# Kernel tuning notes

Hardware: AMD Instinct MI355X
Metric: run time of the kernel (lower is better)

Reference implementation:

```python
import jax, jax.numpy as jnp
import numpy as np

CAT_SIZES = [31360, 6807, 18, 94]
TOTAL = int(sum(CAT_SIZES))          # 38279
EMB = 128
N_FIELDS = len(CAT_SIZES)
D_IN = N_FIELDS * EMB                # 512 (num_features is empty)
MLP_DIMS = [2048, 1024, 512]
B = 16384
OFFSETS = np.concatenate([[0], np.cumsum(CAT_SIZES)[:-1]]).astype(np.int32)


def setup_inputs() -> dict:
    key = jax.random.key(0)
    ks = jax.random.split(key, 20)
    # x holds raw per-field category ids stored as float32 (as the torch model expects)
    cols = [jax.random.randint(ks[i], (B,), 0, s) for i, s in enumerate(CAT_SIZES)]
    x = jnp.stack(cols, axis=1).astype(jnp.float32)

    bias = jnp.zeros((1,), jnp.float32)
    fc = jax.random.uniform(ks[4], (TOTAL, 1), dtype=jnp.float32)          # nn.Parameter(torch.rand)
    emb_table = jax.random.normal(ks[5], (TOTAL, EMB), dtype=jnp.float32)  # nn.Embedding default N(0,1)

    dims = [D_IN] + MLP_DIMS + [1]
    params = {}
    for i in range(len(dims) - 1):
        fan_in = dims[i]
        bound = 1.0 / np.sqrt(fan_in)
        params[f"W{i+1}"] = jax.random.uniform(ks[6 + 2 * i], (dims[i], dims[i + 1]), jnp.float32, -bound, bound)
        params[f"b{i+1}"] = jax.random.uniform(ks[7 + 2 * i], (dims[i + 1],), jnp.float32, -bound, bound)

    return dict(x=x, bias=bias, fc=fc, emb_table=emb_table, **params)


def reference(x, bias, fc, emb_table, W1, b1, W2, b2, W3, b3, W4, b4):
    cat = x.astype(jnp.int32)                       # [B, F] raw per-field ids
    b = cat.shape[0]

    # embedding lookup with RAW (un-offset) ids, faithful to the original code
    embed_x = emb_table[cat].reshape(b, -1)          # [B, F*EMB]

    # one_hot(offset ids) @ fc  ==  sum_f fc[offset ids]  (offset ranges disjoint)
    gidx = cat + jnp.asarray(OFFSETS)                # [B, F] global ids
    lin = jnp.sum(fc[gidx, 0], axis=1)               # [B]
    fm_y = bias + lin                                # [B]

    # FM term: embed_x is 2-D, so sum over dim=1 collapses features;
    # the keepdim sum over dim=-1 then collapses the BATCH dim to shape (1,)
    # (a quirk of the original code that we reproduce exactly)
    square_of_sum = jnp.sum(embed_x, axis=1) ** 2    # [B]
    sum_of_square = jnp.sum(embed_x ** 2, axis=1)    # [B]
    fm_y = fm_y + 0.5 * jnp.sum(square_of_sum - sum_of_square, axis=-1, keepdims=True)  # [B]
    fm_y = fm_y[:, None]                             # [B,1]

    # MLP (eval mode: dropout is identity)
    h = embed_x
    for W, bb in ((W1, b1), (W2, b2), (W3, b3)):
        h = jax.nn.relu(h @ W + bb)
    mlp_y = h @ W4 + b4                              # [B,1]

    return jax.nn.sigmoid(fm_y + mlp_y)              # [B,1]
```

## Files before the change

kernel.cpp:

```cpp
#include <hip/hip_runtime.h>
#include <hip/hip_fp8.h>
#include <cstdint>


typedef float f32x4 __attribute__((ext_vector_type(4)));
typedef int i32x4 __attribute__((ext_vector_type(4)));
typedef int i32x8 __attribute__((ext_vector_type(8)));

#define GLOAD16(gptr, lptr)                                                \
  __builtin_amdgcn_global_load_lds(                                        \
      (const __attribute__((address_space(1))) void*)(gptr),               \
      (__attribute__((address_space(3))) void*)(lptr), 16, 0, 0)

__device__ inline uint32_t f2fp4(float v) {
  uint32_t s = (__float_as_uint(v) >> 31) << 3;
  float a = fabsf(v);
  uint32_t m;
  if (a < 0.25f) m = 0;
  else if (a < 0.75f) m = 1;
  else if (a < 1.25f) m = 2;
  else if (a < 1.75f) m = 3;
  else if (a < 2.5f)  m = 4;
  else if (a < 3.5f)  m = 5;
  else if (a < 5.0f)  m = 6;
  else m = 7;
  return s | m;
}

static constexpr size_t OFF_LIN  = 0;
static constexpr size_t OFF_PART = 65536;
static constexpr size_t OFF_ACC  = 98304;
static constexpr size_t OFF_EMB  = 262144;
static constexpr size_t OFF_H1   = OFF_EMB + 8388608ull;
static constexpr size_t OFF_H2   = OFF_H1 + 33554432ull;
static constexpr size_t OFF_W1T  = OFF_H2 + 16777216ull;
static constexpr size_t OFF_W2T  = OFF_W1T + 524288ull;
static constexpr size_t OFF_W3T  = OFF_W2T + 1048576ull;

__global__ void prep(const float* __restrict__ W1, const float* __restrict__ W2,
                     const float* __restrict__ W3, uint8_t* __restrict__ W1T,
                     uint8_t* __restrict__ W2T, uint8_t* __restrict__ W3T,
                     const float* __restrict__ x, const float* __restrict__ fc,
                     const float* __restrict__ emb, uint8_t* __restrict__ ebf,
                     float* __restrict__ lin, float* __restrict__ partials,
                     float* __restrict__ dotacc) {
  __shared__ __align__(16) float smem[32 * 33];
  int blk = blockIdx.x;
  int tid = threadIdx.x;
  if (blk < 3584) {
    const float* W;
    uint8_t* WT;
    int K, N, bx, by;
    if (blk < 1024) {
      W = W1; WT = W1T; K = 512; N = 2048; bx = blk & 63; by = blk >> 6;
    } else if (blk < 3072) {
      int t = blk - 1024;
      W = W2; WT = W2T; K = 2048; N = 1024; bx = t & 31; by = t >> 5;
    } else {
      int t = blk - 3072;
      W = W3; WT = W3T; K = 1024; N = 512; bx = t & 15; by = t >> 4;
    }
    int tx = tid & 31, ty = tid >> 5;
    int n0 = bx * 32, k0 = by * 32;
#pragma unroll
    for (int i = ty; i < 32; i += 8)
      smem[i * 33 + tx] = W[(size_t)(k0 + i) * N + n0 + tx];
    __syncthreads();
    if (tx < 16) {
#pragma unroll
      for (int i = ty; i < 32; i += 8) {
        uint32_t lo = f2fp4(smem[(2 * tx) * 33 + i] * 128.f);
        uint32_t hi = f2fp4(smem[(2 * tx + 1) * 33 + i] * 128.f);
        WT[(size_t)(n0 + i) * (K >> 1) + (k0 >> 1) + tx] =
            (uint8_t)(lo | (hi << 4));
      }
    }
  } else if (blk < 7680) {
    int gb = blk - 3584;
    int wv = tid >> 6, lane = tid & 63;
    int b = gb * 4 + wv;
    int f = lane >> 4;
    int idx = (int)x[b * 4 + f];
    const float* row = emb + (size_t)idx * 128 + (lane & 15) * 8;
    float4 v0 = ((const float4*)row)[0];
    float4 v1 = ((const float4*)row)[1];
    float s = v0.x + v0.y + v0.z + v0.w + v1.x + v1.y + v1.z + v1.w;
    float q = v0.x * v0.x + v0.y * v0.y + v0.z * v0.z + v0.w * v0.w +
              v1.x * v1.x + v1.y * v1.y + v1.z * v1.z + v1.w * v1.w;

    int lo = 0, hi = 0;
    lo = __builtin_amdgcn_cvt_pk_fp8_f32(v0.x, v0.y, lo, false);
    lo = __builtin_amdgcn_cvt_pk_fp8_f32(v0.z, v0.w, lo, true);
    hi = __builtin_amdgcn_cvt_pk_fp8_f32(v1.x, v1.y, hi, false);
    hi = __builtin_amdgcn_cvt_pk_fp8_f32(v1.z, v1.w, hi, true);
    int2 pk = make_int2(lo, hi);
    *(int2*)(ebf + (size_t)b * 512 + lane * 8) = pk;

    float lp = 0.f;
    if ((lane & 15) == 0) {
      int off = (f == 1) ? 31360 : (f == 2) ? 38167 : (f == 3) ? 38185 : 0;
      lp = fc[idx + off];
    }
#pragma unroll
    for (int m = 32; m; m >>= 1) {
      s += __shfl_xor(s, m);
      q += __shfl_xor(q, m);
      lp += __shfl_xor(lp, m);
    }
    float* pt = smem;
    if (lane == 0) {
      lin[b] = lp;
      pt[wv] = s * s - q;
    }
    __syncthreads();
    if (tid == 0) partials[gb] = pt[0] + pt[1] + pt[2] + pt[3];
  } else {
    int zb = blk - 7680;
    ((float4*)dotacc)[zb * 256 + tid] = make_float4(0.f, 0.f, 0.f, 0.f);
  }
}

__global__ __launch_bounds__(256) void gemm_mx_relu(
    const uint8_t* __restrict__ A, const uint8_t* __restrict__ BT,
    const float* __restrict__ bias, uint8_t* __restrict__ C, int K, int N,
    int GX) {
  __shared__ __align__(16) uint8_t As[128][128];
  __shared__ __align__(16) uint8_t Bs[128][64];
  int bid = blockIdx.x;
  int by = (bid & 7) + ((bid >> 3) / GX) * 8;
  int bx = (bid >> 3) & (GX - 1);
  int tid = threadIdx.x;
  int wv = tid >> 6, lane = tid & 63;
  int m0 = by * 128, n0 = bx * 128;
  int mw = (wv >> 1) * 64, nw = (wv & 1) * 64;
  int ml = lane & 15, kg = lane >> 4;
  int Kb2 = K >> 1;
  int asrow = lane >> 3;
  int ascol = ((lane & 7) ^ asrow) * 16;
  int bsrow = lane >> 2;
  int bscol = ((lane & 3) ^ (bsrow & 3)) * 16;
  int pa0 = ((2 * kg) ^ (ml & 7)) * 16;
  int pa1 = ((2 * kg + 1) ^ (ml & 7)) * 16;
  int pb = (kg ^ (ml & 3)) * 16;

  f32x4 acc[4][4];
#pragma unroll
  for (int i = 0; i < 4; ++i)
#pragma unroll
    for (int j = 0; j < 4; ++j) acc[i][j] = (f32x4){0.f, 0.f, 0.f, 0.f};

  for (int kt = 0; kt < K; kt += 128) {
#pragma unroll
    for (int r = 0; r < 4; ++r) {
      int g = r * 4 + wv;
      const uint8_t* ga = A + (size_t)(m0 + 8 * g + asrow) * K + kt + ascol;
      GLOAD16(ga, &As[8 * g][0]);
    }
#pragma unroll
    for (int r = 0; r < 2; ++r) {
      int g = r * 4 + wv;
      const uint8_t* gb =
          BT + (size_t)(n0 + 16 * g + bsrow) * Kb2 + (kt >> 1) + bscol;
      GLOAD16(gb, &Bs[16 * g][0]);
    }
    __syncthreads();

    i32x4 z = (i32x4){0, 0, 0, 0};
    i32x8 af[4], bfr[4];
#pragma unroll
    for (int t = 0; t < 4; ++t) {
      int ra = mw + t * 16 + ml;
      i32x4 a0 = *(const i32x4*)&As[ra][pa0];
      i32x4 a1 = *(const i32x4*)&As[ra][pa1];
      af[t] = __builtin_shufflevector(a0, a1, 0, 1, 2, 3, 4, 5, 6, 7);
      i32x4 vb = *(const i32x4*)&Bs[nw + t * 16 + ml][pb];
      bfr[t] = __builtin_shufflevector(vb, z, 0, 1, 2, 3, 4, 5, 6, 7);
    }
#pragma unroll
    for (int mt = 0; mt < 4; ++mt)
#pragma unroll
      for (int nt = 0; nt < 4; ++nt)
        acc[mt][nt] = __builtin_amdgcn_mfma_scale_f32_16x16x128_f8f6f4(
            af[mt], bfr[nt], acc[mt][nt],
             0,  4,
            0, 0x7F7F7F7F, 0, 0x78787878);
    __syncthreads();
  }

  int rbase = kg * 4;
#pragma unroll
  for (int nt = 0; nt < 4; ++nt) {
    int col = n0 + nw + nt * 16 + ml;
    float bv = bias[col];
#pragma unroll
    for (int mt = 0; mt < 4; ++mt) {
      int row = m0 + mw + mt * 16 + rbase;
      float v0 = acc[mt][nt][0] + bv, v1 = acc[mt][nt][1] + bv;
      float v2 = acc[mt][nt][2] + bv, v3 = acc[mt][nt][3] + bv;
      v0 = v0 > 0.f ? v0 : 0.f;
      v1 = v1 > 0.f ? v1 : 0.f;
      v2 = v2 > 0.f ? v2 : 0.f;
      v3 = v3 > 0.f ? v3 : 0.f;
      int w01 = __builtin_amdgcn_cvt_pk_fp8_f32(v0, v1, 0, false);
      int w23 = __builtin_amdgcn_cvt_pk_fp8_f32(v2, v3, 0, false);
      C[(size_t)(row + 0) * N + col] = (uint8_t)(w01 & 0xFF);
      C[(size_t)(row + 1) * N + col] = (uint8_t)((w01 >> 8) & 0xFF);
      C[(size_t)(row + 2) * N + col] = (uint8_t)(w23 & 0xFF);
      C[(size_t)(row + 3) * N + col] = (uint8_t)((w23 >> 8) & 0xFF);
    }
  }
}

__global__ __launch_bounds__(256) void gemm_mx_dot(
    const uint8_t* __restrict__ A, const uint8_t* __restrict__ BT,
    const float* __restrict__ bias, const float* __restrict__ W4,
    float* __restrict__ dotacc, int K, int N, int GX) {
  __shared__ __align__(16) uint8_t As[128][128];
  __shared__ __align__(16) uint8_t Bs[128][64];
  int bid = blockIdx.x;
  int by = (bid & 7) + ((bid >> 3) / GX) * 8;
  int bx = (bid >> 3) & (GX - 1);
  int tid = threadIdx.x;
  int wv = tid >> 6, lane = tid & 63;
  int m0 = by * 128, n0 = bx * 128;
  int mw = (wv >> 1) * 64, nw = (wv & 1) * 64;
  int ml = lane & 15, kg = lane >> 4;
  int Kb2 = K >> 1;
  int asrow = lane >> 3;
  int ascol = ((lane & 7) ^ asrow) * 16;
  int bsrow = lane >> 2;
  int bscol = ((lane & 3) ^ (bsrow & 3)) * 16;
  int pa0 = ((2 * kg) ^ (ml & 7)) * 16;
  int pa1 = ((2 * kg + 1) ^ (ml & 7)) * 16;
  int pb = (kg ^ (ml & 3)) * 16;

  f32x4 acc[4][4];
#pragma unroll
  for (int i = 0; i < 4; ++i)
#pragma unroll
    for (int j = 0; j < 4; ++j) acc[i][j] = (f32x4){0.f, 0.f, 0.f, 0.f};

  for (int kt = 0; kt < K; kt += 128) {
#pragma unroll
    for (int r = 0; r < 4; ++r) {
      int g = r * 4 + wv;
      const uint8_t* ga = A + (size_t)(m0 + 8 * g + asrow) * K + kt + ascol;
      GLOAD16(ga, &As[8 * g][0]);
    }
#pragma unroll
    for (int r = 0; r < 2; ++r) {
      int g = r * 4 + wv;
      const uint8_t* gb =
          BT + (size_t)(n0 + 16 * g + bsrow) * Kb2 + (kt >> 1) + bscol;
      GLOAD16(gb, &Bs[16 * g][0]);
    }
    __syncthreads();

    i32x4 z = (i32x4){0, 0, 0, 0};
    i32x8 af[4], bfr[4];
#pragma unroll
    for (int t = 0; t < 4; ++t) {
      int ra = mw + t * 16 + ml;
      i32x4 a0 = *(const i32x4*)&As[ra][pa0];
      i32x4 a1 = *(const i32x4*)&As[ra][pa1];
      af[t] = __builtin_shufflevector(a0, a1, 0, 1, 2, 3, 4, 5, 6, 7);
      i32x4 vb = *(const i32x4*)&Bs[nw + t * 16 + ml][pb];
      bfr[t] = __builtin_shufflevector(vb, z, 0, 1, 2, 3, 4, 5, 6, 7);
    }
#pragma unroll
    for (int mt = 0; mt < 4; ++mt)
#pragma unroll
      for (int nt = 0; nt < 4; ++nt)
        acc[mt][nt] = __builtin_amdgcn_mfma_scale_f32_16x16x128_f8f6f4(
            af[mt], bfr[nt], acc[mt][nt],
            0, 4, 0, 0x7F7F7F7F, 0, 0x78787878);
    __syncthreads();
  }

  float bv[4], w4v[4];
#pragma unroll
  for (int nt = 0; nt < 4; ++nt) {
    int col = n0 + nw + nt * 16 + ml;
    bv[nt] = bias[col];
    w4v[nt] = W4[col];
  }
  int rbase = kg * 4;
#pragma unroll
  for (int mt = 0; mt < 4; ++mt) {
#pragma unroll
    for (int r = 0; r < 4; ++r) {
      float p = 0.f;
#pragma unroll
      for (int nt = 0; nt < 4; ++nt) {
        float v = acc[mt][nt][r] + bv[nt];
        v = v > 0.f ? v : 0.f;
        p += v * w4v[nt];
      }
#pragma unroll
      for (int m = 1; m < 16; m <<= 1) p += __shfl_xor(p, m);
      if (ml == 0)
        atomicAdd(&dotacc[m0 + mw + mt * 16 + rbase + r], p);
    }
  }
}

__global__ void final_out(const float* __restrict__ part,
                          const float* __restrict__ dotacc,
                          const float* __restrict__ lin,
                          const float* __restrict__ bias,
                          const float* __restrict__ b4,
                          float* __restrict__ out) {
  __shared__ float ps[4];
  int tid = threadIdx.x;
  float v = 0.f;
  for (int i = tid; i < 4096; i += 256) v += part[i];
#pragma unroll
  for (int m = 32; m; m >>= 1) v += __shfl_xor(v, m);
  if ((tid & 63) == 0) ps[tid >> 6] = v;
  __syncthreads();
  float S = ps[0] + ps[1] + ps[2] + ps[3];
  int i = blockIdx.x * 256 + tid;
  float z = dotacc[i] + b4[0] + bias[0] + lin[i] + 0.5f * S;
  out[i] = 1.f / (1.f + expf(-z));
}

extern "C" void kernel_launch(void* const* d_in, const int* in_sizes, int n_in,
                              void* d_out, int out_size, void* d_ws,
                              size_t ws_size, hipStream_t stream) {
  const float* x    = (const float*)d_in[0];
  const float* bias = (const float*)d_in[1];
  const float* fc   = (const float*)d_in[2];
  const float* emb  = (const float*)d_in[3];
  const float* W1   = (const float*)d_in[4];
  const float* b1   = (const float*)d_in[5];
  const float* W2   = (const float*)d_in[6];
  const float* b2   = (const float*)d_in[7];
  const float* W3   = (const float*)d_in[8];
  const float* b3   = (const float*)d_in[9];
  const float* W4   = (const float*)d_in[10];
  const float* b4   = (const float*)d_in[11];
  float* out = (float*)d_out;

  char* ws = (char*)d_ws;
  float* lin    = (float*)(ws + OFF_LIN);
  float* part   = (float*)(ws + OFF_PART);
  float* dacc   = (float*)(ws + OFF_ACC);
  uint8_t* EMBb = (uint8_t*)(ws + OFF_EMB);
  uint8_t* H1   = (uint8_t*)(ws + OFF_H1);
  uint8_t* H2   = (uint8_t*)(ws + OFF_H2);
  uint8_t* W1T  = (uint8_t*)(ws + OFF_W1T);
  uint8_t* W2T  = (uint8_t*)(ws + OFF_W2T);
  uint8_t* W3T  = (uint8_t*)(ws + OFF_W3T);

  prep<<<7696, 256, 0, stream>>>(W1, W2, W3, W1T, W2T, W3T, x, fc, emb, EMBb,
                                 lin, part, dacc);

  gemm_mx_relu<<<2048, 256, 0, stream>>>(EMBb, W1T, b1, H1, 512, 2048, 16);
  gemm_mx_relu<<<1024, 256, 0, stream>>>(H1, W2T, b2, H2, 2048, 1024, 8);
  gemm_mx_dot<<<512, 256, 0, stream>>>(H2, W3T, b3, W4, dacc, 1024, 512, 4);

  final_out<<<64, 256, 0, stream>>>(part, dacc, lin, bias, b4, out);
}
```

Baseline: 179.9 us.

## Double-buffer LDS tiles in MX GEMM kernels to overlap loads with MFMA

Both the relu GEMM and the dot GEMM now use two LDS buffers per operand. The first K tile is loaded before the loop, and each iteration issues the global-to-LDS loads for the next tile before running the MFMAs on the current one. This is meant to hide global memory latency behind compute and drop one barrier per iteration. It doubles LDS use per block, which may lower occupancy. It also relies on the end-of-iteration barrier to wait for the async LDS loads.

```diff
diff --git a/kernel.cpp b/kernel.cpp
--- a/kernel.cpp
+++ b/kernel.cpp
@@ -124,8 +124,8 @@
     const uint8_t* __restrict__ A, const uint8_t* __restrict__ BT,
     const float* __restrict__ bias, uint8_t* __restrict__ C, int K, int N,
     int GX) {
-  __shared__ __align__(16) uint8_t As[128][128];
-  __shared__ __align__(16) uint8_t Bs[128][64];
+  __shared__ __align__(16) uint8_t As[2][128][128];
+  __shared__ __align__(16) uint8_t Bs[2][128][64];
   int bid = blockIdx.x;
   int by = (bid & 7) + ((bid >> 3) / GX) * 8;
   int bx = (bid >> 3) & (GX - 1);
@@ -149,31 +149,46 @@
 #pragma unroll
     for (int j = 0; j < 4; ++j) acc[i][j] = (f32x4){0.f, 0.f, 0.f, 0.f};
 
+#pragma unroll
+  for (int r = 0; r < 4; ++r) {
+    int g = r * 4 + wv;
+    GLOAD16(A + (size_t)(m0 + 8 * g + asrow) * K + ascol, &As[0][8 * g][0]);
+  }
+#pragma unroll
+  for (int r = 0; r < 2; ++r) {
+    int g = r * 4 + wv;
+    GLOAD16(BT + (size_t)(n0 + 16 * g + bsrow) * Kb2 + bscol,
+            &Bs[0][16 * g][0]);
+  }
+  __syncthreads();
+
   for (int kt = 0; kt < K; kt += 128) {
-#pragma unroll
-    for (int r = 0; r < 4; ++r) {
-      int g = r * 4 + wv;
-      const uint8_t* ga = A + (size_t)(m0 + 8 * g + asrow) * K + kt + ascol;
-      GLOAD16(ga, &As[8 * g][0]);
-    }
-#pragma unroll
-    for (int r = 0; r < 2; ++r) {
-      int g = r * 4 + wv;
-      const uint8_t* gb =
-          BT + (size_t)(n0 + 16 * g + bsrow) * Kb2 + (kt >> 1) + bscol;
-      GLOAD16(gb, &Bs[16 * g][0]);
-    }
-    __syncthreads();
+    int cur = (kt >> 7) & 1;
+    if (kt + 128 < K) {
+#pragma unroll
+      for (int r = 0; r < 4; ++r) {
+        int g = r * 4 + wv;
+        GLOAD16(A + (size_t)(m0 + 8 * g + asrow) * K + kt + 128 + ascol,
+                &As[cur ^ 1][8 * g][0]);
+      }
+#pragma unroll
+      for (int r = 0; r < 2; ++r) {
+        int g = r * 4 + wv;
+        GLOAD16(BT + (size_t)(n0 + 16 * g + bsrow) * Kb2 + ((kt + 128) >> 1) +
+                    bscol,
+                &Bs[cur ^ 1][16 * g][0]);
+      }
+    }
 
     i32x4 z = (i32x4){0, 0, 0, 0};
     i32x8 af[4], bfr[4];
 #pragma unroll
     for (int t = 0; t < 4; ++t) {
       int ra = mw + t * 16 + ml;
-      i32x4 a0 = *(const i32x4*)&As[ra][pa0];
-      i32x4 a1 = *(const i32x4*)&As[ra][pa1];
+      i32x4 a0 = *(const i32x4*)&As[cur][ra][pa0];
+      i32x4 a1 = *(const i32x4*)&As[cur][ra][pa1];
       af[t] = __builtin_shufflevector(a0, a1, 0, 1, 2, 3, 4, 5, 6, 7);
-      i32x4 vb = *(const i32x4*)&Bs[nw + t * 16 + ml][pb];
+      i32x4 vb = *(const i32x4*)&Bs[cur][nw + t * 16 + ml][pb];
       bfr[t] = __builtin_shufflevector(vb, z, 0, 1, 2, 3, 4, 5, 6, 7);
     }
 #pragma unroll
@@ -215,8 +230,8 @@
     const uint8_t* __restrict__ A, const uint8_t* __restrict__ BT,
     const float* __restrict__ bias, const float* __restrict__ W4,
     float* __restrict__ dotacc, int K, int N, int GX) {
-  __shared__ __align__(16) uint8_t As[128][128];
-  __shared__ __align__(16) uint8_t Bs[128][64];
+  __shared__ __align__(16) uint8_t As[2][128][128];
+  __shared__ __align__(16) uint8_t Bs[2][128][64];
   int bid = blockIdx.x;
   int by = (bid & 7) + ((bid >> 3) / GX) * 8;
   int bx = (bid >> 3) & (GX - 1);
@@ -240,31 +255,46 @@
 #pragma unroll
     for (int j = 0; j < 4; ++j) acc[i][j] = (f32x4){0.f, 0.f, 0.f, 0.f};
 
+#pragma unroll
+  for (int r = 0; r < 4; ++r) {
+    int g = r * 4 + wv;
+    GLOAD16(A + (size_t)(m0 + 8 * g + asrow) * K + ascol, &As[0][8 * g][0]);
+  }
+#pragma unroll
+  for (int r = 0; r < 2; ++r) {
+    int g = r * 4 + wv;
+    GLOAD16(BT + (size_t)(n0 + 16 * g + bsrow) * Kb2 + bscol,
+            &Bs[0][16 * g][0]);
+  }
+  __syncthreads();
+
   for (int kt = 0; kt < K; kt += 128) {
-#pragma unroll
-    for (int r = 0; r < 4; ++r) {
-      int g = r * 4 + wv;
-      const uint8_t* ga = A + (size_t)(m0 + 8 * g + asrow) * K + kt + ascol;
-      GLOAD16(ga, &As[8 * g][0]);
-    }
-#pragma unroll
-    for (int r = 0; r < 2; ++r) {
-      int g = r * 4 + wv;
-      const uint8_t* gb =
-          BT + (size_t)(n0 + 16 * g + bsrow) * Kb2 + (kt >> 1) + bscol;
-      GLOAD16(gb, &Bs[16 * g][0]);
-    }
-    __syncthreads();
+    int cur = (kt >> 7) & 1;
+    if (kt + 128 < K) {
+#pragma unroll
+      for (int r = 0; r < 4; ++r) {
+        int g = r * 4 + wv;
+        GLOAD16(A + (size_t)(m0 + 8 * g + asrow) * K + kt + 128 + ascol,
+                &As[cur ^ 1][8 * g][0]);
+      }
+#pragma unroll
+      for (int r = 0; r < 2; ++r) {
+        int g = r * 4 + wv;
+        GLOAD16(BT + (size_t)(n0 + 16 * g + bsrow) * Kb2 + ((kt + 128) >> 1) +
+                    bscol,
+                &Bs[cur ^ 1][16 * g][0]);
+      }
+    }
 
     i32x4 z = (i32x4){0, 0, 0, 0};
     i32x8 af[4], bfr[4];
 #pragma unroll
     for (int t = 0; t < 4; ++t) {
       int ra = mw + t * 16 + ml;
-      i32x4 a0 = *(const i32x4*)&As[ra][pa0];
-      i32x4 a1 = *(const i32x4*)&As[ra][pa1];
+      i32x4 a0 = *(const i32x4*)&As[cur][ra][pa0];
+      i32x4 a1 = *(const i32x4*)&As[cur][ra][pa1];
       af[t] = __builtin_shufflevector(a0, a1, 0, 1, 2, 3, 4, 5, 6, 7);
-      i32x4 vb = *(const i32x4*)&Bs[nw + t * 16 + ml][pb];
+      i32x4 vb = *(const i32x4*)&Bs[cur][nw + t * 16 + ml][pb];
       bfr[t] = __builtin_shufflevector(vb, z, 0, 1, 2, 3, 4, 5, 6, 7);
     }
 #pragma unroll
```

New measurement: 181.6 us. Within noise of the previous version (+0.9%).
